# Kernel optimization log

Hardware: AMD Instinct MI355X
Metric: run time of the kernel (lower is better)

The kernel has to match this reference:

```python
import jax, jax.numpy as jnp
import numpy as np

LAMBDA_CONE = 0.5   # module-level constant in original repo
TAU_TEMP = 1.0      # softmax temperature
EPS = 1e-8


def setup_inputs() -> dict:
    key = jax.random.key(0)
    k1, k2, k3 = jax.random.split(key, 3)
    B, N, K, D = 8, 32768, 64, 64
    features = jax.random.normal(k1, (B, N, D), dtype=jnp.float32)
    slots = jax.random.normal(k2, (B, K, D), dtype=jnp.float32)
    horizons = jax.random.uniform(k3, (B, K), dtype=jnp.float32)  # positive horizons
    return {"features": features, "slots": slots, "horizons": horizons}


def _pairwise_minkowski(features, slots):
    # Minkowski split: channel 0 is time-like, channels 1: are space-like.
    ft, fs = features[..., 0], features[..., 1:]   # [B,N], [B,N,D-1]
    st, ss = slots[..., 0], slots[..., 1:]          # [B,K], [B,K,D-1]
    # dt[b,k,n] = t_feat - t_slot
    dt = ft[:, None, :] - st[:, :, None]            # [B,K,N]
    # squared spatial distance via the expansion ||f-s||^2 = ||f||^2 - 2 f.s + ||s||^2
    # (avoids materializing a [B,K,N,D] difference tensor)
    cross = jnp.einsum('bnd,bkd->bkn', fs, ss)      # [B,K,N]
    dx2 = (fs * fs).sum(-1)[:, None, :] - 2.0 * cross + (ss * ss).sum(-1)[:, :, None]
    dx2 = jnp.maximum(dx2, 0.0)                     # guard tiny negatives from expansion
    return dt, dx2


def reference(features, slots, horizons):
    dt, dx2 = _pairwise_minkowski(features, slots)  # [B,K,N] each
    # proper-time interval s^2 = dt^2 - |dx|^2; signed sqrt as the safe distance
    interval = dt * dt - dx2
    dist = jnp.sign(interval) * jnp.sqrt(jnp.abs(interval) + EPS)
    # cone score: how deep inside the light cone, scaled by per-slot horizon
    cone = (jnp.abs(dt) - jnp.sqrt(dx2 + EPS)) / (horizons[:, :, None] + EPS)
    logits = (-jnp.abs(dist) + jnp.tanh(cone) * LAMBDA_CONE) / TAU_TEMP
    attention = jax.nn.softmax(logits, axis=1)      # softmax over slots
    return attention
```

## Files before the change

kernel.cpp:

```cpp
#include <hip/hip_runtime.h>
#include <math.h>

#define EPSF 1e-8f

typedef _Float16 f16x8 __attribute__((ext_vector_type(8)));
typedef float    f32x4 __attribute__((ext_vector_type(4)));

constexpr int Bb = 8, Nn = 32768, Kk = 64, Dd = 64;

__global__ __launch_bounds__(256, 4) void attn_kernel(
    const float* __restrict__ features,
    const float* __restrict__ slots,
    const float* __restrict__ horizons,
    float* __restrict__ out)
{
    __shared__ float s_st[Kk], s_ss2[Kk], s_rh[Kk];
    __shared__ f16x8 s_ahi[8][64];
    __shared__ f16x8 s_alo[8][64];

    const int tid  = threadIdx.x;
    const int bid  = blockIdx.x;
    const int b    = bid >> 8;
    const int blk  = bid & 255;
    const int lane = tid & 63;
    const int wid  = tid >> 6;
    const int m    = lane & 15;
    const int quad = lane >> 4;

    if (tid < Kk) {
        const float4* sr = (const float4*)(slots + (size_t)(b * Kk + tid) * Dd);
        float4 v = sr[0];
        float st = v.x;
        float ss = v.y * v.y + v.z * v.z + v.w * v.w;
        #pragma unroll
        for (int i = 1; i < 16; ++i) {
            float4 u = sr[i];
            ss += u.x * u.x + u.y * u.y + u.z * u.z + u.w * u.w;
        }
        s_st[tid]  = st;
        s_ss2[tid] = ss;
        s_rh[tid]  = 1.0f / (horizons[b * Kk + tid] + EPSF);
    }

    {
        const int t = wid;
        #pragma unroll
        for (int c = 0; c < 2; ++c) {
            const float* sp = slots + (size_t)(b * Kk + 16 * t + m) * Dd
                            + 32 * c + quad * 8;
            float4 u0 = *(const float4*)sp;
            float4 u1 = *(const float4*)(sp + 4);
            float fv[8] = {u0.x, u0.y, u0.z, u0.w, u1.x, u1.y, u1.z, u1.w};
            if (c == 0 && quad == 0) fv[0] = 0.0f;
            f16x8 h8, l8;
            #pragma unroll
            for (int j = 0; j < 8; ++j) {
                float x = fv[j];
                _Float16 h = (_Float16)x;
                _Float16 l = (_Float16)(x - (float)h);
                h8[j] = h;
                l8[j] = l;
            }
            s_ahi[t * 2 + c][lane] = h8;
            s_alo[t * 2 + c][lane] = l8;
        }
    }
    __syncthreads();

    const int base_tile = blk * 8 + wid * 2;

    float4 buf[2][4];
    {
        const float* fp0 = features + (((size_t)b << 15) + (size_t)base_tile * 16 + m) * Dd
                         + quad * 8;
        buf[0][0] = *(const float4*)(fp0);
        buf[0][1] = *(const float4*)(fp0 + 4);
        buf[0][2] = *(const float4*)(fp0 + 32);
        buf[0][3] = *(const float4*)(fp0 + 36);
    }

    #pragma unroll
    for (int it = 0; it < 2; ++it) {
        if (it == 0) {
            const float* fpn = features + (((size_t)b << 15) + (size_t)(base_tile + 1) * 16 + m) * Dd
                             + quad * 8;
            buf[1][0] = *(const float4*)(fpn);
            buf[1][1] = *(const float4*)(fpn + 4);
            buf[1][2] = *(const float4*)(fpn + 32);
            buf[1][3] = *(const float4*)(fpn + 36);
        }
        const int n0 = (base_tile + it) * 16;

        f16x8 b_hi[2], b_lo[2];
        const float f00 = buf[it][0].x;
        float fs2p = 0.f;
        #pragma unroll
        for (int c = 0; c < 2; ++c) {
            float4 u0 = buf[it][2 * c];
            float4 u1 = buf[it][2 * c + 1];
            float fv[8] = {u0.x, u0.y, u0.z, u0.w, u1.x, u1.y, u1.z, u1.w};
            #pragma unroll
            for (int j = 0; j < 8; ++j) {
                float x = fv[j];
                fs2p = fmaf(x, x, fs2p);
                _Float16 h = (_Float16)x;
                _Float16 l = (_Float16)(x - (float)h);
                b_hi[c][j] = h;
                b_lo[c][j] = l;
            }
        }
        const float ft = __shfl(f00, m);
        float fs2 = fs2p;
        fs2 += __shfl_xor(fs2, 16);
        fs2 += __shfl_xor(fs2, 32);
        fs2 = fmaf(-ft, ft, fs2);

        f32x4 acc[4];
        #pragma unroll
        for (int t = 0; t < 4; ++t) {
            f16x8 ah0 = s_ahi[t * 2 + 0][lane];
            f16x8 ah1 = s_ahi[t * 2 + 1][lane];
            f16x8 al0 = s_alo[t * 2 + 0][lane];
            f16x8 al1 = s_alo[t * 2 + 1][lane];
            f32x4 a = {0.f, 0.f, 0.f, 0.f};
            a = __builtin_amdgcn_mfma_f32_16x16x32_f16(ah0, b_hi[0], a, 0, 0, 0);
            a = __builtin_amdgcn_mfma_f32_16x16x32_f16(ah0, b_lo[0], a, 0, 0, 0);
            a = __builtin_amdgcn_mfma_f32_16x16x32_f16(al0, b_hi[0], a, 0, 0, 0);
            a = __builtin_amdgcn_mfma_f32_16x16x32_f16(ah1, b_hi[1], a, 0, 0, 0);
            a = __builtin_amdgcn_mfma_f32_16x16x32_f16(ah1, b_lo[1], a, 0, 0, 0);
            a = __builtin_amdgcn_mfma_f32_16x16x32_f16(al1, b_hi[1], a, 0, 0, 0);
            acc[t] = a;
        }

        float sum = 0.f;
        #pragma unroll
        for (int t = 0; t < 4; ++t) {
            #pragma unroll
            for (int r = 0; r < 4; ++r) {
                const int k = 16 * t + quad * 4 + r;
                float st  = s_st[k];
                float ss2 = s_ss2[k];
                float rh  = s_rh[k];
                float cross = acc[t][r];
                float dt  = ft - st;
                float dx2 = fmaf(-2.f, cross, fs2 + ss2);
                dx2 = fmaxf(dx2, 0.f);
                float interval = fmaf(dt, dt, -dx2);
                float adist = __builtin_amdgcn_sqrtf(fabsf(interval) + EPSF);
                float cone  = (fabsf(dt) - __builtin_amdgcn_sqrtf(dx2 + EPSF)) * rh;
                float e  = __expf(2.0f * cone);
                float th = 1.0f - 2.0f * __builtin_amdgcn_rcpf(e + 1.0f);
                float logit = fmaf(0.5f, th, -adist);
                float pe = __expf(logit);
                acc[t][r] = pe;
                sum += pe;
            }
        }
        sum += __shfl_xor(sum, 16);
        sum += __shfl_xor(sum, 32);
        const float inv = __builtin_amdgcn_rcpf(sum);

        float* ob = out + (((size_t)(b * Kk)) << 15) + n0 + m;
        #pragma unroll
        for (int t = 0; t < 4; ++t) {
            #pragma unroll
            for (int r = 0; r < 4; ++r) {
                const int k = 16 * t + quad * 4 + r;
                ob[(size_t)k << 15] = acc[t][r] * inv;
            }
        }
    }
}

extern "C" void kernel_launch(void* const* d_in, const int* in_sizes, int n_in,
                              void* d_out, int out_size, void* d_ws, size_t ws_size,
                              hipStream_t stream) {
    const float* features = (const float*)d_in[0];
    const float* slots    = (const float*)d_in[1];
    const float* horizons = (const float*)d_in[2];
    float* out = (float*)d_out;

    hipLaunchKernelGGL(attn_kernel, dim3(2048), dim3(256), 0, stream,
                       features, slots, horizons, out);
}
```

Measured before the change: 127.2 us.

## Process both feature tiles jointly to share slot fragments and packed per-slot params

Restructures each wave to convert both 16-row feature tiles up front, then runs the MFMA loop with each slot A-fragment loaded from LDS once and used for both tiles. The epilogue also handles both tiles together. Per-slot constants are packed into one float4 so a single LDS read replaces three. This raises register pressure, so launch bounds drop from 4 to 3 blocks per CU, which may cost occupancy and some latency hiding for memory.

```diff
diff --git a/kernel.cpp b/kernel.cpp
--- a/kernel.cpp
+++ b/kernel.cpp
@@ -8,13 +8,13 @@
 
 constexpr int Bb = 8, Nn = 32768, Kk = 64, Dd = 64;
 
-__global__ __launch_bounds__(256, 4) void attn_kernel(
+__global__ __launch_bounds__(256, 3) void attn_kernel(
     const float* __restrict__ features,
     const float* __restrict__ slots,
     const float* __restrict__ horizons,
     float* __restrict__ out)
 {
-    __shared__ float s_st[Kk], s_ss2[Kk], s_rh[Kk];
+    __shared__ float4 s_kp[Kk];
     __shared__ f16x8 s_ahi[8][64];
     __shared__ f16x8 s_alo[8][64];
 
@@ -37,9 +37,7 @@
             float4 u = sr[i];
             ss += u.x * u.x + u.y * u.y + u.z * u.z + u.w * u.w;
         }
-        s_st[tid]  = st;
-        s_ss2[tid] = ss;
-        s_rh[tid]  = 1.0f / (horizons[b * Kk + tid] + EPSF);
+        s_kp[tid] = make_float4(st, ss, 1.0f / (horizons[b * Kk + tid] + EPSF), 0.f);
     }
 
     {
@@ -68,32 +66,25 @@
     __syncthreads();
 
     const int base_tile = blk * 8 + wid * 2;
+    const int n0 = base_tile * 16;
 
     float4 buf[2][4];
-    {
-        const float* fp0 = features + (((size_t)b << 15) + (size_t)base_tile * 16 + m) * Dd
-                         + quad * 8;
-        buf[0][0] = *(const float4*)(fp0);
-        buf[0][1] = *(const float4*)(fp0 + 4);
-        buf[0][2] = *(const float4*)(fp0 + 32);
-        buf[0][3] = *(const float4*)(fp0 + 36);
+    #pragma unroll
+    for (int it = 0; it < 2; ++it) {
+        const float* fp = features + (((size_t)b << 15) + n0 + it * 16 + m) * Dd
+                        + quad * 8;
+        buf[it][0] = *(const float4*)(fp);
+        buf[it][1] = *(const float4*)(fp + 4);
+        buf[it][2] = *(const float4*)(fp + 32);
+        buf[it][3] = *(const float4*)(fp + 36);
     }
 
+    f16x8 bh[2][2], bl[2][2];
+    float ft0, ft1, fs20, fs21;
     #pragma unroll
     for (int it = 0; it < 2; ++it) {
-        if (it == 0) {
-            const float* fpn = features + (((size_t)b << 15) + (size_t)(base_tile + 1) * 16 + m) * Dd
-                             + quad * 8;
-            buf[1][0] = *(const float4*)(fpn);
-            buf[1][1] = *(const float4*)(fpn + 4);
-            buf[1][2] = *(const float4*)(fpn + 32);
-            buf[1][3] = *(const float4*)(fpn + 36);
-        }
-        const int n0 = (base_tile + it) * 16;
-
-        f16x8 b_hi[2], b_lo[2];
         const float f00 = buf[it][0].x;
-        float fs2p = 0.f;
+        float s = 0.f;
         #pragma unroll
         for (int c = 0; c < 2; ++c) {
             float4 u0 = buf[it][2 * c];
@@ -102,72 +93,82 @@
             #pragma unroll
             for (int j = 0; j < 8; ++j) {
                 float x = fv[j];
-                fs2p = fmaf(x, x, fs2p);
+                s = fmaf(x, x, s);
                 _Float16 h = (_Float16)x;
                 _Float16 l = (_Float16)(x - (float)h);
-                b_hi[c][j] = h;
-                b_lo[c][j] = l;
+                bh[it][c][j] = h;
+                bl[it][c][j] = l;
             }
         }
-        const float ft = __shfl(f00, m);
-        float fs2 = fs2p;
-        fs2 += __shfl_xor(fs2, 16);
-        fs2 += __shfl_xor(fs2, 32);
-        fs2 = fmaf(-ft, ft, fs2);
+        float f = __shfl(f00, m);
+        s += __shfl_xor(s, 16);
+        s += __shfl_xor(s, 32);
+        s = fmaf(-f, f, s);
+        if (it == 0) { ft0 = f; fs20 = s; } else { ft1 = f; fs21 = s; }
+    }
 
-        f32x4 acc[4];
+    f32x4 acc[2][4];
+    #pragma unroll
+    for (int t = 0; t < 4; ++t) {
+        f16x8 ah0 = s_ahi[t * 2 + 0][lane];
+        f16x8 ah1 = s_ahi[t * 2 + 1][lane];
+        f16x8 al0 = s_alo[t * 2 + 0][lane];
+        f16x8 al1 = s_alo[t * 2 + 1][lane];
         #pragma unroll
-        for (int t = 0; t < 4; ++t) {
-            f16x8 ah0 = s_ahi[t * 2 + 0][lane];
-            f16x8 ah1 = s_ahi[t * 2 + 1][lane];
-            f16x8 al0 = s_alo[t * 2 + 0][lane];
-            f16x8 al1 = s_alo[t * 2 + 1][lane];
+        for (int it = 0; it < 2; ++it) {
             f32x4 a = {0.f, 0.f, 0.f, 0.f};
-            a = __builtin_amdgcn_mfma_f32_16x16x32_f16(ah0, b_hi[0], a, 0, 0, 0);
-            a = __builtin_amdgcn_mfma_f32_16x16x32_f16(ah0, b_lo[0], a, 0, 0, 0);
-            a = __builtin_amdgcn_mfma_f32_16x16x32_f16(al0, b_hi[0], a, 0, 0, 0);
-            a = __builtin_amdgcn_mfma_f32_16x16x32_f16(ah1, b_hi[1], a, 0, 0, 0);
-            a = __builtin_amdgcn_mfma_f32_16x16x32_f16(ah1, b_lo[1], a, 0, 0, 0);
-            a = __builtin_amdgcn_mfma_f32_16x16x32_f16(al1, b_hi[1], a, 0, 0, 0);
-            acc[t] = a;
+            a = __builtin_amdgcn_mfma_f32_16x16x32_f16(ah0, bh[it][0], a, 0, 0, 0);
+            a = __builtin_amdgcn_mfma_f32_16x16x32_f16(ah0, bl[it][0], a, 0, 0, 0);
+            a = __builtin_amdgcn_mfma_f32_16x16x32_f16(al0, bh[it][0], a, 0, 0, 0);
+            a = __builtin_amdgcn_mfma_f32_16x16x32_f16(ah1, bh[it][1], a, 0, 0, 0);
+            a = __builtin_amdgcn_mfma_f32_16x16x32_f16(ah1, bl[it][1], a, 0, 0, 0);
+            a = __builtin_amdgcn_mfma_f32_16x16x32_f16(al1, bh[it][1], a, 0, 0, 0);
+            acc[it][t] = a;
         }
+    }
 
-        float sum = 0.f;
+    float sum0 = 0.f, sum1 = 0.f;
+    #pragma unroll
+    for (int t = 0; t < 4; ++t) {
         #pragma unroll
-        for (int t = 0; t < 4; ++t) {
+        for (int r = 0; r < 4; ++r) {
+            const int k = 16 * t + quad * 4 + r;
+            float4 kp = s_kp[k];
             #pragma unroll
-            for (int r = 0; r < 4; ++r) {
-                const int k = 16 * t + quad * 4 + r;
-                float st  = s_st[k];
-                float ss2 = s_ss2[k];
-                float rh  = s_rh[k];
-                float cross = acc[t][r];
-                float dt  = ft - st;
-                float dx2 = fmaf(-2.f, cross, fs2 + ss2);
+            for (int it = 0; it < 2; ++it) {
+                float cross = acc[it][t][r];
+                float ftv = (it == 0) ? ft0 : ft1;
+                float fsv = (it == 0) ? fs20 : fs21;
+                float dt  = ftv - kp.x;
+                float dx2 = fmaf(-2.f, cross, fsv + kp.y);
                 dx2 = fmaxf(dx2, 0.f);
                 float interval = fmaf(dt, dt, -dx2);
                 float adist = __builtin_amdgcn_sqrtf(fabsf(interval) + EPSF);
-                float cone  = (fabsf(dt) - __builtin_amdgcn_sqrtf(dx2 + EPSF)) * rh;
+                float cone  = (fabsf(dt) - __builtin_amdgcn_sqrtf(dx2 + EPSF)) * kp.z;
                 float e  = __expf(2.0f * cone);
                 float th = 1.0f - 2.0f * __builtin_amdgcn_rcpf(e + 1.0f);
                 float logit = fmaf(0.5f, th, -adist);
                 float pe = __expf(logit);
-                acc[t][r] = pe;
-                sum += pe;
+                acc[it][t][r] = pe;
+                if (it == 0) sum0 += pe; else sum1 += pe;
             }
         }
-        sum += __shfl_xor(sum, 16);
-        sum += __shfl_xor(sum, 32);
-        const float inv = __builtin_amdgcn_rcpf(sum);
+    }
+    sum0 += __shfl_xor(sum0, 16);
+    sum0 += __shfl_xor(sum0, 32);
+    sum1 += __shfl_xor(sum1, 16);
+    sum1 += __shfl_xor(sum1, 32);
+    const float inv0 = __builtin_amdgcn_rcpf(sum0);
+    const float inv1 = __builtin_amdgcn_rcpf(sum1);
 
-        float* ob = out + (((size_t)(b * Kk)) << 15) + n0 + m;
+    float* ob = out + (((size_t)(b * Kk)) << 15) + n0 + m;
+    #pragma unroll
+    for (int t = 0; t < 4; ++t) {
         #pragma unroll
-        for (int t = 0; t < 4; ++t) {
-            #pragma unroll
-            for (int r = 0; r < 4; ++r) {
-                const int k = 16 * t + quad * 4 + r;
-                ob[(size_t)k << 15] = acc[t][r] * inv;
-            }
+        for (int r = 0; r < 4; ++r) {
+            const int k = 16 * t + quad * 4 + r;
+            ob[(size_t)k << 15]        = acc[0][t][r] * inv0;
+            ob[((size_t)k << 15) + 16] = acc[1][t][r] * inv1;
         }
     }
 }
```

After: 125.3 us. No clear change (-1.5%).

## Process one tile per wave and double grid size; pack slot params into float4

Applied to the files above, without the earlier changes.

Each wave now handles a single 16-column tile instead of two, removing the manual prefetch of the second tile, and the grid doubles to 4096 blocks with a launch-bounds occupancy hint of 5. Per-slot constants are packed into one float4 in shared memory so each slot needs a single LDS load. The intent is more waves in flight to hide global memory latency on this bandwidth-bound kernel. In exchange, the per-block setup work (slot fp16 split and norms) is repeated twice as often, and the explicit in-wave prefetch overlap is lost.

```diff
diff --git a/kernel.cpp b/kernel.cpp
--- a/kernel.cpp
+++ b/kernel.cpp
@@ -8,20 +8,20 @@
 
 constexpr int Bb = 8, Nn = 32768, Kk = 64, Dd = 64;
 
-__global__ __launch_bounds__(256, 4) void attn_kernel(
+__global__ __launch_bounds__(256, 5) void attn_kernel(
     const float* __restrict__ features,
     const float* __restrict__ slots,
     const float* __restrict__ horizons,
     float* __restrict__ out)
 {
-    __shared__ float s_st[Kk], s_ss2[Kk], s_rh[Kk];
+    __shared__ float4 s_kp[Kk];
     __shared__ f16x8 s_ahi[8][64];
     __shared__ f16x8 s_alo[8][64];
 
     const int tid  = threadIdx.x;
     const int bid  = blockIdx.x;
-    const int b    = bid >> 8;
-    const int blk  = bid & 255;
+    const int b    = bid >> 9;
+    const int blk  = bid & 511;
     const int lane = tid & 63;
     const int wid  = tid >> 6;
     const int m    = lane & 15;
@@ -29,17 +29,15 @@
 
     if (tid < Kk) {
         const float4* sr = (const float4*)(slots + (size_t)(b * Kk + tid) * Dd);
-        float4 v = sr[0];
-        float st = v.x;
-        float ss = v.y * v.y + v.z * v.z + v.w * v.w;
-        #pragma unroll
-        for (int i = 1; i < 16; ++i) {
+        float st = 0.f, ss = 0.f;
+        #pragma unroll 4
+        for (int i = 0; i < 16; ++i) {
             float4 u = sr[i];
+            if (i == 0) st = u.x;
             ss += u.x * u.x + u.y * u.y + u.z * u.z + u.w * u.w;
         }
-        s_st[tid]  = st;
-        s_ss2[tid] = ss;
-        s_rh[tid]  = 1.0f / (horizons[b * Kk + tid] + EPSF);
+        ss -= st * st;
+        s_kp[tid] = make_float4(st, ss, 1.0f / (horizons[b * Kk + tid] + EPSF), 0.f);
     }
 
     {
@@ -67,107 +65,90 @@
     }
     __syncthreads();
 
-    const int base_tile = blk * 8 + wid * 2;
+    const int n0 = (blk * 4 + wid) * 16;
 
-    float4 buf[2][4];
+    float4 buf[4];
     {
-        const float* fp0 = features + (((size_t)b << 15) + (size_t)base_tile * 16 + m) * Dd
-                         + quad * 8;
-        buf[0][0] = *(const float4*)(fp0);
-        buf[0][1] = *(const float4*)(fp0 + 4);
-        buf[0][2] = *(const float4*)(fp0 + 32);
-        buf[0][3] = *(const float4*)(fp0 + 36);
+        const float* fp = features + (((size_t)b << 15) + n0 + m) * Dd + quad * 8;
+        buf[0] = *(const float4*)(fp);
+        buf[1] = *(const float4*)(fp + 4);
+        buf[2] = *(const float4*)(fp + 32);
+        buf[3] = *(const float4*)(fp + 36);
     }
 
+    f16x8 bh[2], bl[2];
+    const float f00 = buf[0].x;
+    float fs2 = 0.f;
     #pragma unroll
-    for (int it = 0; it < 2; ++it) {
-        if (it == 0) {
-            const float* fpn = features + (((size_t)b << 15) + (size_t)(base_tile + 1) * 16 + m) * Dd
-                             + quad * 8;
-            buf[1][0] = *(const float4*)(fpn);
-            buf[1][1] = *(const float4*)(fpn + 4);
-            buf[1][2] = *(const float4*)(fpn + 32);
-            buf[1][3] = *(const float4*)(fpn + 36);
+    for (int c = 0; c < 2; ++c) {
+        float4 u0 = buf[2 * c];
+        float4 u1 = buf[2 * c + 1];
+        float fv[8] = {u0.x, u0.y, u0.z, u0.w, u1.x, u1.y, u1.z, u1.w};
+        #pragma unroll
+        for (int j = 0; j < 8; ++j) {
+            float x = fv[j];
+            fs2 = fmaf(x, x, fs2);
+            _Float16 h = (_Float16)x;
+            _Float16 l = (_Float16)(x - (float)h);
+            bh[c][j] = h;
+            bl[c][j] = l;
         }
-        const int n0 = (base_tile + it) * 16;
+    }
+    const float ft = __shfl(f00, m);
+    fs2 += __shfl_xor(fs2, 16);
+    fs2 += __shfl_xor(fs2, 32);
+    fs2 = fmaf(-ft, ft, fs2);
 
-        f16x8 b_hi[2], b_lo[2];
-        const float f00 = buf[it][0].x;
-        float fs2p = 0.f;
+    f32x4 acc[4];
+    #pragma unroll
+    for (int t = 0; t < 4; ++t) {
+        f16x8 ah0 = s_ahi[t * 2 + 0][lane];
+        f16x8 ah1 = s_ahi[t * 2 + 1][lane];
+        f16x8 al0 = s_alo[t * 2 + 0][lane];
+        f16x8 al1 = s_alo[t * 2 + 1][lane];
+        f32x4 a = {0.f, 0.f, 0.f, 0.f};
+        a = __builtin_amdgcn_mfma_f32_16x16x32_f16(ah0, bh[0], a, 0, 0, 0);
+        a = __builtin_amdgcn_mfma_f32_16x16x32_f16(ah0, bl[0], a, 0, 0, 0);
+        a = __builtin_amdgcn_mfma_f32_16x16x32_f16(al0, bh[0], a, 0, 0, 0);
+        a = __builtin_amdgcn_mfma_f32_16x16x32_f16(ah1, bh[1], a, 0, 0, 0);
+        a = __builtin_amdgcn_mfma_f32_16x16x32_f16(ah1, bl[1], a, 0, 0, 0);
+        a = __builtin_amdgcn_mfma_f32_16x16x32_f16(al1, bh[1], a, 0, 0, 0);
+        acc[t] = a;
+    }
+
+    float sum = 0.f;
+    #pragma unroll
+    for (int t = 0; t < 4; ++t) {
         #pragma unroll
-        for (int c = 0; c < 2; ++c) {
-            float4 u0 = buf[it][2 * c];
-            float4 u1 = buf[it][2 * c + 1];
-            float fv[8] = {u0.x, u0.y, u0.z, u0.w, u1.x, u1.y, u1.z, u1.w};
-            #pragma unroll
-            for (int j = 0; j < 8; ++j) {
-                float x = fv[j];
-                fs2p = fmaf(x, x, fs2p);
-                _Float16 h = (_Float16)x;
-                _Float16 l = (_Float16)(x - (float)h);
-                b_hi[c][j] = h;
-                b_lo[c][j] = l;
-            }
+        for (int r = 0; r < 4; ++r) {
+            const int k = 16 * t + quad * 4 + r;
+            float4 kp = s_kp[k];
+            float cross = acc[t][r];
+            float dt  = ft - kp.x;
+            float dx2 = fmaf(-2.f, cross, fs2 + kp.y);
+            dx2 = fmaxf(dx2, 0.f);
+            float interval = fmaf(dt, dt, -dx2);
+            float adist = __builtin_amdgcn_sqrtf(fabsf(interval) + EPSF);
+            float cone  = (fabsf(dt) - __builtin_amdgcn_sqrtf(dx2 + EPSF)) * kp.z;
+            float e  = __expf(2.0f * cone);
+            float th = 1.0f - 2.0f * __builtin_amdgcn_rcpf(e + 1.0f);
+            float logit = fmaf(0.5f, th, -adist);
+            float pe = __expf(logit);
+            acc[t][r] = pe;
+            sum += pe;
         }
-        const float ft = __shfl(f00, m);
-        float fs2 = fs2p;
-        fs2 += __shfl_xor(fs2, 16);
-        fs2 += __shfl_xor(fs2, 32);
-        fs2 = fmaf(-ft, ft, fs2);
+    }
+    sum += __shfl_xor(sum, 16);
+    sum += __shfl_xor(sum, 32);
+    const float inv = __builtin_amdgcn_rcpf(sum);
 
-        f32x4 acc[4];
+    float* ob = out + (((size_t)(b * Kk)) << 15) + n0 + m;
+    #pragma unroll
+    for (int t = 0; t < 4; ++t) {
         #pragma unroll
-        for (int t = 0; t < 4; ++t) {
-            f16x8 ah0 = s_ahi[t * 2 + 0][lane];
-            f16x8 ah1 = s_ahi[t * 2 + 1][lane];
-            f16x8 al0 = s_alo[t * 2 + 0][lane];
-            f16x8 al1 = s_alo[t * 2 + 1][lane];
-            f32x4 a = {0.f, 0.f, 0.f, 0.f};
-            a = __builtin_amdgcn_mfma_f32_16x16x32_f16(ah0, b_hi[0], a, 0, 0, 0);
-            a = __builtin_amdgcn_mfma_f32_16x16x32_f16(ah0, b_lo[0], a, 0, 0, 0);
-            a = __builtin_amdgcn_mfma_f32_16x16x32_f16(al0, b_hi[0], a, 0, 0, 0);
-            a = __builtin_amdgcn_mfma_f32_16x16x32_f16(ah1, b_hi[1], a, 0, 0, 0);
-            a = __builtin_amdgcn_mfma_f32_16x16x32_f16(ah1, b_lo[1], a, 0, 0, 0);
-            a = __builtin_amdgcn_mfma_f32_16x16x32_f16(al1, b_hi[1], a, 0, 0, 0);
-            acc[t] = a;
-        }
-
-        float sum = 0.f;
-        #pragma unroll
-        for (int t = 0; t < 4; ++t) {
-            #pragma unroll
-            for (int r = 0; r < 4; ++r) {
-                const int k = 16 * t + quad * 4 + r;
-                float st  = s_st[k];
-                float ss2 = s_ss2[k];
-                float rh  = s_rh[k];
-                float cross = acc[t][r];
-                float dt  = ft - st;
-                float dx2 = fmaf(-2.f, cross, fs2 + ss2);
-                dx2 = fmaxf(dx2, 0.f);
-                float interval = fmaf(dt, dt, -dx2);
-                float adist = __builtin_amdgcn_sqrtf(fabsf(interval) + EPSF);
-                float cone  = (fabsf(dt) - __builtin_amdgcn_sqrtf(dx2 + EPSF)) * rh;
-                float e  = __expf(2.0f * cone);
-                float th = 1.0f - 2.0f * __builtin_amdgcn_rcpf(e + 1.0f);
-                float logit = fmaf(0.5f, th, -adist);
-                float pe = __expf(logit);
-                acc[t][r] = pe;
-                sum += pe;
-            }
-        }
-        sum += __shfl_xor(sum, 16);
-        sum += __shfl_xor(sum, 32);
-        const float inv = __builtin_amdgcn_rcpf(sum);
-
-        float* ob = out + (((size_t)(b * Kk)) << 15) + n0 + m;
-        #pragma unroll
-        for (int t = 0; t < 4; ++t) {
-            #pragma unroll
-            for (int r = 0; r < 4; ++r) {
-                const int k = 16 * t + quad * 4 + r;
-                ob[(size_t)k << 15] = acc[t][r] * inv;
-            }
+        for (int r = 0; r < 4; ++r) {
+            const int k = 16 * t + quad * 4 + r;
+            ob[(size_t)k << 15] = acc[t][r] * inv;
         }
     }
 }
@@ -180,6 +161,6 @@
     const float* horizons = (const float*)d_in[2];
     float* out = (float*)d_out;
 
-    hipLaunchKernelGGL(attn_kernel, dim3(2048), dim3(256), 0, stream,
+    hipLaunchKernelGGL(attn_kernel, dim3(4096), dim3(256), 0, stream,
                        features, slots, horizons, out);
 }
```

After: 133.5 us. +4.9%, slower.
